# Kernel tuning notes

Hardware: AMD Instinct MI355X
Metric: run time of the kernel (lower is better)

## Reference

```python
import jax, jax.numpy as jnp
import numpy as np

B, N, D = 2, 128, 512  # batch, tokens, embed_dim (= in_features = out_features)
LAYERS = 3


def setup_inputs() -> dict:
    key = jax.random.key(0)
    ks = jax.random.split(key, 9)
    s = lambda fan_in: 1.0 / np.sqrt(fan_in)
    return {
        "text_embedding": jax.random.normal(ks[0], (B, N, D), dtype=jnp.float32),
        # weights stored as [in, out] so y = x @ W + b (matches torch Linear math)
        "W_rel": jax.random.uniform(ks[1], (2 * D, D), jnp.float32, -s(2 * D), s(2 * D)),
        "b_rel": jax.random.uniform(ks[2], (D,), jnp.float32, -s(2 * D), s(2 * D)),
        "W_go": jax.random.uniform(ks[3], (D, D), jnp.float32, -s(D), s(D)),
        "b_go": jax.random.uniform(ks[4], (D,), jnp.float32, -s(D), s(D)),
        "W_gr": jax.random.uniform(ks[5], (3 * D, D), jnp.float32, -s(3 * D), s(3 * D)),
        "b_gr": jax.random.uniform(ks[6], (D,), jnp.float32, -s(3 * D), s(3 * D)),
        "W_esa": jax.random.uniform(ks[7], (D, D), jnp.float32, -s(D), s(D)),
        "b_esa": jax.random.uniform(ks[8], (D,), jnp.float32, -s(D), s(D)),
    }


def reference(text_embedding, W_rel, b_rel, W_go, b_go, W_gr, b_gr, W_esa, b_esa):
    x = text_embedding  # [B, N, D]
    n = x.shape[1]
    rel = None
    for i in range(LAYERS):
        new_x = jnp.tanh(x @ W_go + b_go)  # [B, N, D]
        # pairwise broadcast-concat: [B, N, N, 2D]
        a = jnp.broadcast_to(x[:, :, None, :], (x.shape[0], n, n, x.shape[-1]))
        b = jnp.broadcast_to(x[:, None, :, :], (x.shape[0], n, n, x.shape[-1]))
        rlf = jnp.concatenate([a, b], axis=3)
        if i == 0:
            rel = rlf @ W_rel + b_rel  # [B, N, N, D]
        rlf2 = jnp.concatenate([rlf, rel], axis=3)  # [B, N, N, 3D]
        rel = jnp.tanh(rlf2 @ W_gr + b_gr)  # [B, N, N, D]
        x = new_x
    rel = rel @ W_esa + b_esa  # [B, N, N, D]
    # original subtracts max over dim=1 then applies Softmax(dim=1); equivalent to stable softmax over axis 1
    attn = jax.nn.softmax(rel, axis=1)
    rel_out = jnp.sum(attn * rel, axis=-2)  # sum over second N axis -> [B, N, D]
    return (x, rel_out)
```

## Files before the change

### kernel.cpp

```cpp
#include <hip/hip_runtime.h>
#include <hip/hip_bf16.h>
#include <stdint.h>


#define DEV static __device__ __forceinline__

typedef float  f32x4   __attribute__((ext_vector_type(4)));
typedef float  f32x16  __attribute__((ext_vector_type(16)));
typedef __bf16 bf16x8  __attribute__((ext_vector_type(8)));
typedef __bf16 bf16x4  __attribute__((ext_vector_type(4)));

DEV float tanh_fast(float x) {
  float e = __expf(2.0f * x);
  return 1.0f - 2.0f * __frcp_rn(e + 1.0f);
}

DEV void gl_lds16(const void* g, void* l) {
  __builtin_amdgcn_global_load_lds(
      (const __attribute__((address_space(1))) unsigned int*)g,
      (__attribute__((address_space(3))) unsigned int*)l, 16, 0, 0);
}

struct WC { const float* W; __bf16* Wh; __bf16* Wl; };
struct Prep {
  WC w[7];
  const float* x0; __bf16* x0h; __bf16* x0l;
  const float* b_rel; const float* Wgrc; const float* b_gr; float* dvec;
};

__global__ __launch_bounds__(256) void prep_kernel(Prep pp) {
  const int y = blockIdx.y;
  if (y < 7) {
    const WC wc = pp.w[y];
    __shared__ float tile[32][33];
    int t = threadIdx.x;
    int tx = t & 31, ty = t >> 5;
    int bx = blockIdx.x & 15, by = blockIdx.x >> 4;
    int k0 = by * 32, n0 = bx * 32;
#pragma unroll
    for (int r = 0; r < 4; ++r) {
      int k = ty + r * 8;
      tile[k][tx] = wc.W[(size_t)(k0 + k) * 512 + n0 + tx];
    }
    __syncthreads();
#pragma unroll
    for (int r = 0; r < 4; ++r) {
      int n = ty + r * 8;
      float v = tile[tx][n];
      __bf16 h = (__bf16)v;
      wc.Wh[(size_t)(n0 + n) * 512 + k0 + tx] = h;
      wc.Wl[(size_t)(n0 + n) * 512 + k0 + tx] = (__bf16)(v - (float)h);
    }
  } else if (y == 7) {
    int i = blockIdx.x * 256 + threadIdx.x;
    if (i < 32768) {
      float4 v = ((const float4*)pp.x0)[i];
      float vv[4] = {v.x, v.y, v.z, v.w};
      bf16x4 h, l;
#pragma unroll
      for (int e = 0; e < 4; ++e) {
        __bf16 he = (__bf16)vv[e];
        h[e] = he;
        l[e] = (__bf16)(vv[e] - (float)he);
      }
      ((bf16x4*)pp.x0h)[i] = h;
      ((bf16x4*)pp.x0l)[i] = l;
    }
  } else {
    if (blockIdx.x < 2) {
      int n = blockIdx.x * 256 + threadIdx.x;
      float acc = pp.b_gr[n];
#pragma unroll 8
      for (int k = 0; k < 512; ++k) acc += pp.b_rel[k] * pp.Wgrc[(size_t)k * 512 + n];
      pp.dvec[n] = acc;
    }
  }
}

struct MOp {
  const __bf16* Xh; const __bf16* Xl;
  const __bf16* Wh; const __bf16* Wl;
  const float* bias;
  const float* add;
  float* outf;
  __bf16* outh; __bf16* outl;
  int act;
};
struct MBatch { MOp op[5]; };

__global__ __launch_bounds__(256, 2) void mfma_small_kernel(MBatch batch) {
  const MOp o = batch.op[blockIdx.y];
  const int m0 = ((int)blockIdx.x >> 3) * 64;
  const int n0 = ((int)blockIdx.x & 7) * 64;
  __shared__ __bf16 Ah[64 * 64], Al[64 * 64], Bh[64 * 64], Bl[64 * 64];
  const int t = threadIdx.x, lane = t & 63, wave = t >> 6;
  const int waveM = wave >> 1, waveN = wave & 1;
  const bool comp = (o.Xl != nullptr);

  f32x4 vzero = {0.f, 0.f, 0.f, 0.f};
  f32x4 acc[2][2];
#pragma unroll
  for (int a = 0; a < 2; ++a)
#pragma unroll
    for (int c = 0; c < 2; ++c) acc[a][c] = vzero;

  const int lr = lane >> 3, lc = (lane & 7) * 8;

  for (int k0 = 0; k0 < 512; k0 += 64) {
    __syncthreads();
#pragma unroll
    for (int r = 0; r < 2; ++r) {
      const int rb = r * 32 + wave * 8;
      gl_lds16(o.Xh + (size_t)(m0 + rb + lr) * 512 + k0 + lc, &Ah[rb * 64]);
      gl_lds16(o.Wh + (size_t)(n0 + rb + lr) * 512 + k0 + lc, &Bh[rb * 64]);
      if (comp) {
        gl_lds16(o.Xl + (size_t)(m0 + rb + lr) * 512 + k0 + lc, &Al[rb * 64]);
        gl_lds16(o.Wl + (size_t)(n0 + rb + lr) * 512 + k0 + lc, &Bl[rb * 64]);
      }
    }
    __syncthreads();
#pragma unroll
    for (int kk = 0; kk < 2; ++kk) {
      const int koff = kk * 32 + (lane >> 4) * 8;
      const int ml = lane & 15;
      bf16x8 ah[2], bh[2], al[2], bl[2];
#pragma unroll
      for (int tm = 0; tm < 2; ++tm)
        ah[tm] = *(const bf16x8*)&Ah[(waveM * 32 + tm * 16 + ml) * 64 + koff];
#pragma unroll
      for (int tn = 0; tn < 2; ++tn)
        bh[tn] = *(const bf16x8*)&Bh[(waveN * 32 + tn * 16 + ml) * 64 + koff];
      if (comp) {
#pragma unroll
        for (int tm = 0; tm < 2; ++tm)
          al[tm] = *(const bf16x8*)&Al[(waveM * 32 + tm * 16 + ml) * 64 + koff];
#pragma unroll
        for (int tn = 0; tn < 2; ++tn)
          bl[tn] = *(const bf16x8*)&Bl[(waveN * 32 + tn * 16 + ml) * 64 + koff];
      }
#pragma unroll
      for (int tm = 0; tm < 2; ++tm)
#pragma unroll
        for (int tn = 0; tn < 2; ++tn) {
          acc[tm][tn] = __builtin_amdgcn_mfma_f32_16x16x32_bf16(ah[tm], bh[tn], acc[tm][tn], 0, 0, 0);
          if (comp) {
            acc[tm][tn] = __builtin_amdgcn_mfma_f32_16x16x32_bf16(ah[tm], bl[tn], acc[tm][tn], 0, 0, 0);
            acc[tm][tn] = __builtin_amdgcn_mfma_f32_16x16x32_bf16(al[tm], bh[tn], acc[tm][tn], 0, 0, 0);
          }
        }
    }
  }

  const int quad = lane >> 4, cl = lane & 15;
#pragma unroll
  for (int tm = 0; tm < 2; ++tm) {
#pragma unroll
    for (int r = 0; r < 4; ++r) {
      const int row = m0 + waveM * 32 + tm * 16 + quad * 4 + r;
#pragma unroll
      for (int tn = 0; tn < 2; ++tn) {
        const int col = n0 + waveN * 32 + tn * 16 + cl;
        float v = acc[tm][tn][r];
        if (o.bias) v += o.bias[col];
        if (o.add) v += o.add[(size_t)row * 512 + col];
        if (o.act) v = tanh_fast(v);
        if (o.outf) o.outf[(size_t)row * 512 + col] = v;
        if (o.outh) {
          __bf16 h = (__bf16)v;
          o.outh[(size_t)row * 512 + col] = h;
          o.outl[(size_t)row * 512 + col] = (__bf16)(v - (float)h);
        }
      }
    }
  }
}

__global__ __launch_bounds__(256) void rel1_kernel(
    const float* __restrict__ A, const float* __restrict__ C,
    __bf16* __restrict__ R1) {
  size_t e = ((size_t)blockIdx.x * 256 + threadIdx.x) * 8;
  int d = (int)(e & 511);
  int j = (int)((e >> 9) & 127);
  int bi = (int)(e >> 16);
  int b = bi >> 7;
  const float* ap = &A[(size_t)bi * 512 + d];
  const float* cp = &C[((size_t)(b * 128 + j)) * 512 + d];
  float av[8], cv[8];
  *(float4*)&av[0] = *(const float4*)ap;
  *(float4*)&av[4] = *(const float4*)(ap + 4);
  *(float4*)&cv[0] = *(const float4*)cp;
  *(float4*)&cv[4] = *(const float4*)(cp + 4);
  bf16x8 o;
#pragma unroll
  for (int k = 0; k < 8; ++k) o[k] = (__bf16)tanh_fast(av[k] + cv[k]);
  *(bf16x8*)&R1[e] = o;
}

constexpr int BM = 128, BN = 128, BK = 64;
DEV int lds_off(int row) { return row * 64 + (row >> 3) * 8; }

template <int MODE>
__global__ __launch_bounds__(256, 2) void big_gemm_kernel(
    const __bf16* __restrict__ Ab, const __bf16* __restrict__ Wt,
    const float* __restrict__ P, const float* __restrict__ Q,
    const float* __restrict__ bias, __bf16* __restrict__ outb,
    float* __restrict__ outf) {
  __shared__ __bf16 As[BM * BK + 16 * 8];
  __shared__ __bf16 Bs[BN * BK + 16 * 8];
  const int t = threadIdx.x;
  const int lane = t & 63;
  const int wave = t >> 6;
  const int blk = ((int)blockIdx.x & 7) * 128 + ((int)blockIdx.x >> 3);
  const int bm = blk >> 2;
  const int n0 = (blk & 3) * BN;
  const size_t r0 = (size_t)bm * BM;
  const int b = bm >> 7;
  const int i = bm & 127;
  const int waveM = wave >> 1, waveN = wave & 1;

  f32x16 acc[2][2];
#pragma unroll
  for (int a = 0; a < 2; ++a)
#pragma unroll
    for (int c = 0; c < 2; ++c) acc[a][c] = (f32x16)0.f;

  for (int k0 = 0; k0 < 512; k0 += BK) {
    __syncthreads();
#pragma unroll
    for (int p2 = 0; p2 < 4; ++p2) {
      int rowg = wave * 32 + p2 * 8;
      const __bf16* ga = Ab + (r0 + rowg + (lane >> 3)) * 512 + k0 + (lane & 7) * 8;
      gl_lds16(ga, &As[lds_off(rowg)]);
      const __bf16* gb = Wt + (size_t)(n0 + rowg + (lane >> 3)) * 512 + k0 + (lane & 7) * 8;
      gl_lds16(gb, &Bs[lds_off(rowg)]);
    }
    __syncthreads();
    const int ml = lane & 31;
    const int kl = (lane >> 5) * 8;
#pragma unroll
    for (int ks = 0; ks < 4; ++ks) {
      const int koff = ks * 16 + kl;
      bf16x8 af[2], bfr[2];
#pragma unroll
      for (int tm = 0; tm < 2; ++tm)
        af[tm] = *(const bf16x8*)&As[lds_off(waveM * 64 + tm * 32 + ml) + koff];
#pragma unroll
      for (int tn = 0; tn < 2; ++tn)
        bfr[tn] = *(const bf16x8*)&Bs[lds_off(waveN * 64 + tn * 32 + ml) + koff];
#pragma unroll
      for (int tm = 0; tm < 2; ++tm)
#pragma unroll
        for (int tn = 0; tn < 2; ++tn)
          acc[tm][tn] = __builtin_amdgcn_mfma_f32_32x32x16_bf16(af[tm], bfr[tn], acc[tm][tn], 0, 0, 0);
    }
  }

  const int cl = lane & 31, lg = lane >> 5;
#pragma unroll
  for (int tm = 0; tm < 2; ++tm) {
#pragma unroll
    for (int tn = 0; tn < 2; ++tn) {
      const int col = n0 + waveN * 64 + tn * 32 + cl;
      float pv;
      if (MODE == 2) pv = bias[col];
      else pv = P[((size_t)(b * 128 + i)) * 512 + col];
#pragma unroll
      for (int reg = 0; reg < 16; ++reg) {
        const int row = waveM * 64 + tm * 32 + (reg & 3) + 8 * (reg >> 2) + 4 * lg;
        float v = acc[tm][tn][reg] + pv;
        if (MODE == 2) {
          outf[(r0 + row) * 512 + col] = v;
        } else {
          v += Q[((size_t)(b * 128 + row)) * 512 + col];
          outb[(r0 + row) * 512 + col] = (__bf16)tanh_fast(v);
        }
      }
    }
  }
}

__global__ __launch_bounds__(256) void softmax_l_kernel(
    const float* __restrict__ S, float* __restrict__ Lb) {
  int idx = blockIdx.x * 256 + threadIdx.x;
  int d = idx & 511;
  int j = (idx >> 9) & 127;
  int b = idx >> 16;
  const float* p = S + ((size_t)b * 16384 + j) * 512 + d;
  float l = 0.f;
#pragma unroll 8
  for (int ii = 0; ii < 128; ++ii) l += __expf(p[(size_t)ii * 65536]);
  Lb[idx] = __frcp_rn(l);
}

__global__ __launch_bounds__(256) void softmax_out_kernel(
    const float* __restrict__ S, const float* __restrict__ Lb,
    float* __restrict__ outp) {
  int idx = blockIdx.x * 256 + threadIdx.x;
  int d = idx & 511;
  int i = (idx >> 9) & 127;
  int b = idx >> 16;
  const float* sp = S + ((size_t)(b * 128 + i)) * 65536 + d;
  const float* lp = Lb + (size_t)b * 65536 + d;
  float acc = 0.f;
#pragma unroll 8
  for (int jj = 0; jj < 128; ++jj) {
    float s = sp[(size_t)jj * 512];
    acc += __expf(s) * lp[(size_t)jj * 512] * s;
  }
  outp[idx] = acc;
}

extern "C" void kernel_launch(void* const* d_in, const int* in_sizes, int n_in,
                              void* d_out, int out_size, void* d_ws, size_t ws_size,
                              hipStream_t stream) {
  const float* x0    = (const float*)d_in[0];
  const float* W_rel = (const float*)d_in[1];
  const float* b_rel = (const float*)d_in[2];
  const float* W_go  = (const float*)d_in[3];
  const float* b_go  = (const float*)d_in[4];
  const float* W_gr  = (const float*)d_in[5];
  const float* b_gr  = (const float*)d_in[6];
  const float* W_esa = (const float*)d_in[7];
  const float* b_esa = (const float*)d_in[8];

  const float* Wrel_top = W_rel;
  const float* Wrel_bot = W_rel + 512 * 512;
  const float* Wgr_a = W_gr;
  const float* Wgr_b = W_gr + 512 * 512;
  const float* Wgr_c = W_gr + 2 * 512 * 512;

  char* ws = (char*)d_ws;
  size_t off = 0;
  auto alloc = [&](size_t bytes) -> void* {
    void* p = ws + off;
    off += (bytes + 255) & ~(size_t)255;
    return p;
  };
  const size_t NREL = 16777216ull;
  float*  S  = (float*)alloc(NREL * 4);
  __bf16* R1 = (__bf16*)alloc(NREL * 2);
  __bf16* R2 = (__bf16*)alloc(NREL * 2);
  float* p0t  = (float*)alloc(131072 * 4);
  float* q0t  = (float*)alloc(131072 * 4);
  float* Abuf = (float*)alloc(131072 * 4);
  float* Cbuf = (float*)alloc(131072 * 4);
  float* p1   = (float*)alloc(131072 * 4);
  float* q1   = (float*)alloc(131072 * 4);
  float* p2   = (float*)alloc(131072 * 4);
  float* q2   = (float*)alloc(131072 * 4);
  float* dvec = (float*)alloc(512 * 4);
  float* Lb   = (float*)alloc(131072 * 4);
  __bf16* x0h = (__bf16*)alloc(131072 * 2);
  __bf16* x0l = (__bf16*)alloc(131072 * 2);
  __bf16* x1h = (__bf16*)alloc(131072 * 2);
  __bf16* x1l = (__bf16*)alloc(131072 * 2);
  __bf16* x2h = (__bf16*)alloc(131072 * 2);
  __bf16* x2l = (__bf16*)alloc(131072 * 2);
  __bf16* u0h = (__bf16*)alloc(131072 * 2);
  __bf16* u0l = (__bf16*)alloc(131072 * 2);
  __bf16* v0h = (__bf16*)alloc(131072 * 2);
  __bf16* v0l = (__bf16*)alloc(131072 * 2);
  __bf16* Wgo_h = (__bf16*)alloc(262144 * 2);
  __bf16* Wgo_l = (__bf16*)alloc(262144 * 2);
  __bf16* Wrt_h = (__bf16*)alloc(262144 * 2);
  __bf16* Wrt_l = (__bf16*)alloc(262144 * 2);
  __bf16* Wrb_h = (__bf16*)alloc(262144 * 2);
  __bf16* Wrb_l = (__bf16*)alloc(262144 * 2);
  __bf16* Wga_h = (__bf16*)alloc(262144 * 2);
  __bf16* Wga_l = (__bf16*)alloc(262144 * 2);
  __bf16* Wgb_h = (__bf16*)alloc(262144 * 2);
  __bf16* Wgb_l = (__bf16*)alloc(262144 * 2);
  __bf16* Wgc_h = (__bf16*)alloc(262144 * 2);
  __bf16* Wgc_l = (__bf16*)alloc(262144 * 2);
  __bf16* Wes_h = (__bf16*)alloc(262144 * 2);
  __bf16* Wes_l = (__bf16*)alloc(262144 * 2);

  float* x3out  = (float*)d_out;
  float* relout = (float*)d_out + 131072;

  Prep pp;
  pp.w[0] = {W_go, Wgo_h, Wgo_l};
  pp.w[1] = {Wrel_top, Wrt_h, Wrt_l};
  pp.w[2] = {Wrel_bot, Wrb_h, Wrb_l};
  pp.w[3] = {Wgr_a, Wga_h, Wga_l};
  pp.w[4] = {Wgr_b, Wgb_h, Wgb_l};
  pp.w[5] = {Wgr_c, Wgc_h, Wgc_l};
  pp.w[6] = {W_esa, Wes_h, Wes_l};
  pp.x0 = x0; pp.x0h = x0h; pp.x0l = x0l;
  pp.b_rel = b_rel; pp.Wgrc = Wgr_c; pp.b_gr = b_gr; pp.dvec = dvec;
  prep_kernel<<<dim3(256, 9), 256, 0, stream>>>(pp);

  MBatch m1 = {};
  m1.op[0] = {x0h, x0l, Wgo_h, Wgo_l, b_go, nullptr, nullptr, x1h, x1l, 1};
  m1.op[1] = {x0h, x0l, Wrt_h, Wrt_l, nullptr, nullptr, nullptr, u0h, u0l, 0};
  m1.op[2] = {x0h, x0l, Wrb_h, Wrb_l, nullptr, nullptr, nullptr, v0h, v0l, 0};
  m1.op[3] = {x0h, x0l, Wga_h, Wga_l, nullptr, nullptr, p0t, nullptr, nullptr, 0};
  m1.op[4] = {x0h, x0l, Wgb_h, Wgb_l, nullptr, nullptr, q0t, nullptr, nullptr, 0};
  mfma_small_kernel<<<dim3(32, 5), 256, 0, stream>>>(m1);

  MBatch m2 = {};
  m2.op[0] = {x1h, x1l, Wgo_h, Wgo_l, b_go, nullptr, nullptr, x2h, x2l, 1};
  m2.op[1] = {u0h, u0l, Wgc_h, Wgc_l, dvec, p0t, Abuf, nullptr, nullptr, 0};
  m2.op[2] = {v0h, v0l, Wgc_h, Wgc_l, nullptr, q0t, Cbuf, nullptr, nullptr, 0};
  m2.op[3] = {x1h, x1l, Wga_h, Wga_l, b_gr, nullptr, p1, nullptr, nullptr, 0};
  m2.op[4] = {x1h, x1l, Wgb_h, Wgb_l, nullptr, nullptr, q1, nullptr, nullptr, 0};
  mfma_small_kernel<<<dim3(32, 5), 256, 0, stream>>>(m2);

  MBatch m3 = {};
  m3.op[0] = {x2h, x2l, Wgo_h, Wgo_l, b_go, nullptr, x3out, nullptr, nullptr, 1};
  m3.op[1] = {x2h, x2l, Wga_h, Wga_l, b_gr, nullptr, p2, nullptr, nullptr, 0};
  m3.op[2] = {x2h, x2l, Wgb_h, Wgb_l, nullptr, nullptr, q2, nullptr, nullptr, 0};
  mfma_small_kernel<<<dim3(32, 3), 256, 0, stream>>>(m3);

  rel1_kernel<<<8192, 256, 0, stream>>>(Abuf, Cbuf, R1);

  big_gemm_kernel<1><<<1024, 256, 0, stream>>>(R1, Wgc_h, p1, q1, nullptr, R2, nullptr);
  big_gemm_kernel<1><<<1024, 256, 0, stream>>>(R2, Wgc_h, p2, q2, nullptr, R1, nullptr);
  big_gemm_kernel<2><<<1024, 256, 0, stream>>>(R1, Wes_h, nullptr, nullptr, b_esa, nullptr, S);

  softmax_l_kernel<<<512, 256, 0, stream>>>(S, Lb);
  softmax_out_kernel<<<512, 256, 0, stream>>>(S, Lb, relout);
}
```

Before: 261.9 us.

## Double-buffer LDS tiles in both MFMA GEMM kernels to overlap loads with compute

```diff
diff --git a/kernel.cpp b/kernel.cpp
--- a/kernel.cpp
+++ b/kernel.cpp
@@ -92,10 +92,21 @@
   const MOp o = batch.op[blockIdx.y];
   const int m0 = ((int)blockIdx.x >> 3) * 64;
   const int n0 = ((int)blockIdx.x & 7) * 64;
-  __shared__ __bf16 Ah[64 * 64], Al[64 * 64], Bh[64 * 64], Bl[64 * 64];
+  __shared__ __bf16 Ah[2][64 * 64], Al[2][64 * 64], Bh[2][64 * 64], Bl[2][64 * 64];
   const int t = threadIdx.x, lane = t & 63, wave = t >> 6;
   const int waveM = wave >> 1, waveN = wave & 1;
-  const bool comp = (o.Xl != nullptr);
+  const int lr = lane >> 3, lc = (lane & 7) * 8;
+
+  auto stage = [&](int k0, int sel) {
+#pragma unroll
+    for (int r = 0; r < 2; ++r) {
+      const int rb = r * 32 + wave * 8;
+      gl_lds16(o.Xh + (size_t)(m0 + rb + lr) * 512 + k0 + lc, &Ah[sel][rb * 64]);
+      gl_lds16(o.Wh + (size_t)(n0 + rb + lr) * 512 + k0 + lc, &Bh[sel][rb * 64]);
+      gl_lds16(o.Xl + (size_t)(m0 + rb + lr) * 512 + k0 + lc, &Al[sel][rb * 64]);
+      gl_lds16(o.Wl + (size_t)(n0 + rb + lr) * 512 + k0 + lc, &Bl[sel][rb * 64]);
+    }
+  };
 
   f32x4 vzero = {0.f, 0.f, 0.f, 0.f};
   f32x4 acc[2][2];
@@ -104,21 +115,18 @@
 #pragma unroll
     for (int c = 0; c < 2; ++c) acc[a][c] = vzero;
 
-  const int lr = lane >> 3, lc = (lane & 7) * 8;
-
-  for (int k0 = 0; k0 < 512; k0 += 64) {
-    __syncthreads();
-#pragma unroll
-    for (int r = 0; r < 2; ++r) {
-      const int rb = r * 32 + wave * 8;
-      gl_lds16(o.Xh + (size_t)(m0 + rb + lr) * 512 + k0 + lc, &Ah[rb * 64]);
-      gl_lds16(o.Wh + (size_t)(n0 + rb + lr) * 512 + k0 + lc, &Bh[rb * 64]);
-      if (comp) {
-        gl_lds16(o.Xl + (size_t)(m0 + rb + lr) * 512 + k0 + lc, &Al[rb * 64]);
-        gl_lds16(o.Wl + (size_t)(n0 + rb + lr) * 512 + k0 + lc, &Bl[rb * 64]);
-      }
-    }
-    __syncthreads();
+  stage(0, 0);
+#pragma unroll 1
+  for (int kt = 0; kt < 8; ++kt) {
+    const int sel = kt & 1;
+    if (kt < 7) {
+      stage((kt + 1) * 64, sel ^ 1);
+      asm volatile("s_waitcnt vmcnt(8)" ::: "memory");
+    } else {
+      asm volatile("s_waitcnt vmcnt(0)" ::: "memory");
+    }
+    __builtin_amdgcn_s_barrier();
+    __builtin_amdgcn_sched_barrier(0);
 #pragma unroll
     for (int kk = 0; kk < 2; ++kk) {
       const int koff = kk * 32 + (lane >> 4) * 8;
@@ -126,29 +134,26 @@
       bf16x8 ah[2], bh[2], al[2], bl[2];
 #pragma unroll
       for (int tm = 0; tm < 2; ++tm)
-        ah[tm] = *(const bf16x8*)&Ah[(waveM * 32 + tm * 16 + ml) * 64 + koff];
+        ah[tm] = *(const bf16x8*)&Ah[sel][(waveM * 32 + tm * 16 + ml) * 64 + koff];
 #pragma unroll
       for (int tn = 0; tn < 2; ++tn)
-        bh[tn] = *(const bf16x8*)&Bh[(waveN * 32 + tn * 16 + ml) * 64 + koff];
-      if (comp) {
-#pragma unroll
-        for (int tm = 0; tm < 2; ++tm)
-          al[tm] = *(const bf16x8*)&Al[(waveM * 32 + tm * 16 + ml) * 64 + koff];
-#pragma unroll
-        for (int tn = 0; tn < 2; ++tn)
-          bl[tn] = *(const bf16x8*)&Bl[(waveN * 32 + tn * 16 + ml) * 64 + koff];
-      }
+        bh[tn] = *(const bf16x8*)&Bh[sel][(waveN * 32 + tn * 16 + ml) * 64 + koff];
+#pragma unroll
+      for (int tm = 0; tm < 2; ++tm)
+        al[tm] = *(const bf16x8*)&Al[sel][(waveM * 32 + tm * 16 + ml) * 64 + koff];
+#pragma unroll
+      for (int tn = 0; tn < 2; ++tn)
+        bl[tn] = *(const bf16x8*)&Bl[sel][(waveN * 32 + tn * 16 + ml) * 64 + koff];
 #pragma unroll
       for (int tm = 0; tm < 2; ++tm)
 #pragma unroll
         for (int tn = 0; tn < 2; ++tn) {
           acc[tm][tn] = __builtin_amdgcn_mfma_f32_16x16x32_bf16(ah[tm], bh[tn], acc[tm][tn], 0, 0, 0);
-          if (comp) {
-            acc[tm][tn] = __builtin_amdgcn_mfma_f32_16x16x32_bf16(ah[tm], bl[tn], acc[tm][tn], 0, 0, 0);
-            acc[tm][tn] = __builtin_amdgcn_mfma_f32_16x16x32_bf16(al[tm], bh[tn], acc[tm][tn], 0, 0, 0);
-          }
+          acc[tm][tn] = __builtin_amdgcn_mfma_f32_16x16x32_bf16(ah[tm], bl[tn], acc[tm][tn], 0, 0, 0);
+          acc[tm][tn] = __builtin_amdgcn_mfma_f32_16x16x32_bf16(al[tm], bh[tn], acc[tm][tn], 0, 0, 0);
         }
     }
+    __builtin_amdgcn_s_barrier();
   }
 
   const int quad = lane >> 4, cl = lane & 15;
@@ -205,8 +210,8 @@
     const float* __restrict__ P, const float* __restrict__ Q,
     const float* __restrict__ bias, __bf16* __restrict__ outb,
     float* __restrict__ outf) {
-  __shared__ __bf16 As[BM * BK + 16 * 8];
-  __shared__ __bf16 Bs[BN * BK + 16 * 8];
+  __shared__ __bf16 As[2][BM * BK + 16 * 8];
+  __shared__ __bf16 Bs[2][BN * BK + 16 * 8];
   const int t = threadIdx.x;
   const int lane = t & 63;
   const int wave = t >> 6;
@@ -218,23 +223,35 @@
   const int i = bm & 127;
   const int waveM = wave >> 1, waveN = wave & 1;
 
-  f32x16 acc[2][2];
-#pragma unroll
-  for (int a = 0; a < 2; ++a)
-#pragma unroll
-    for (int c = 0; c < 2; ++c) acc[a][c] = (f32x16)0.f;
-
-  for (int k0 = 0; k0 < 512; k0 += BK) {
-    __syncthreads();
+  auto stage = [&](int k0, int sel) {
 #pragma unroll
     for (int p2 = 0; p2 < 4; ++p2) {
       int rowg = wave * 32 + p2 * 8;
       const __bf16* ga = Ab + (r0 + rowg + (lane >> 3)) * 512 + k0 + (lane & 7) * 8;
-      gl_lds16(ga, &As[lds_off(rowg)]);
+      gl_lds16(ga, &As[sel][lds_off(rowg)]);
       const __bf16* gb = Wt + (size_t)(n0 + rowg + (lane >> 3)) * 512 + k0 + (lane & 7) * 8;
-      gl_lds16(gb, &Bs[lds_off(rowg)]);
-    }
-    __syncthreads();
+      gl_lds16(gb, &Bs[sel][lds_off(rowg)]);
+    }
+  };
+
+  f32x16 acc[2][2];
+#pragma unroll
+  for (int a = 0; a < 2; ++a)
+#pragma unroll
+    for (int c = 0; c < 2; ++c) acc[a][c] = (f32x16)0.f;
+
+  stage(0, 0);
+#pragma unroll 1
+  for (int kt = 0; kt < 8; ++kt) {
+    const int sel = kt & 1;
+    if (kt < 7) {
+      stage((kt + 1) * BK, sel ^ 1);
+      asm volatile("s_waitcnt vmcnt(8)" ::: "memory");
+    } else {
+      asm volatile("s_waitcnt vmcnt(0)" ::: "memory");
+    }
+    __builtin_amdgcn_s_barrier();
+    __builtin_amdgcn_sched_barrier(0);
     const int ml = lane & 31;
     const int kl = (lane >> 5) * 8;
 #pragma unroll
@@ -243,16 +260,17 @@
       bf16x8 af[2], bfr[2];
 #pragma unroll
       for (int tm = 0; tm < 2; ++tm)
-        af[tm] = *(const bf16x8*)&As[lds_off(waveM * 64 + tm * 32 + ml) + koff];
+        af[tm] = *(const bf16x8*)&As[sel][lds_off(waveM * 64 + tm * 32 + ml) + koff];
 #pragma unroll
       for (int tn = 0; tn < 2; ++tn)
-        bfr[tn] = *(const bf16x8*)&Bs[lds_off(waveN * 64 + tn * 32 + ml) + koff];
+        bfr[tn] = *(const bf16x8*)&Bs[sel][lds_off(waveN * 64 + tn * 32 + ml) + koff];
 #pragma unroll
       for (int tm = 0; tm < 2; ++tm)
 #pragma unroll
         for (int tn = 0; tn < 2; ++tn)
           acc[tm][tn] = __builtin_amdgcn_mfma_f32_32x32x16_bf16(af[tm], bfr[tn], acc[tm][tn], 0, 0, 0);
     }
+    __builtin_amdgcn_s_barrier();
   }
 
   const int cl = lane & 31, lg = lane >> 5;
```

New measurement: 264.3 us. About the same (+0.9%).
